# Performance work log

Measured on AMD Instinct MI355X. Metric: run time of the kernel, lower is better.

Reference implementation:

```python
import jax, jax.numpy as jnp
from jax import lax
import numpy as np

DIM = 384
HEADS = 8
SR = 2
B, D0, D1, D2 = 4, 16, 16, 16
N = 1 + D0 * D1 * D2


def setup_inputs() -> dict:
    key = jax.random.key(0)
    ks = jax.random.split(key, 8)
    s = 0.02
    return {
        "x": jax.random.normal(ks[0], (B, N, DIM), dtype=jnp.float32),
        "q_w": jax.random.normal(ks[1], (DIM, DIM), dtype=jnp.float32) * s,
        "kv_w": jax.random.normal(ks[2], (2 * DIM, DIM), dtype=jnp.float32) * s,
        "proj_w": jax.random.normal(ks[3], (DIM, DIM), dtype=jnp.float32) * s,
        "proj_b": jnp.zeros((DIM,), dtype=jnp.float32),
        "sr_w": jax.random.normal(ks[4], (DIM, 1, SR, SR, SR), dtype=jnp.float32) * s,  # depthwise (groups=dim)
        "sr_b": jnp.zeros((DIM,), dtype=jnp.float32),
        "ln_g": jnp.ones((DIM,), dtype=jnp.float32),
        "ln_b": jnp.zeros((DIM,), dtype=jnp.float32),
        "d0": D0, "d1": D1, "d2": D2,
    }


def reference(x, q_w, kv_w, proj_w, proj_b, sr_w, sr_b, ln_g, ln_b, d0, d1, d2):
    B_, N_, C = x.shape
    hd = C // HEADS
    scale = hd ** -0.5

    # q projection -> [B, H, N, hd]
    q = (x @ q_w.T).reshape(B_, N_, HEADS, hd).transpose(0, 2, 1, 3)

    # spatial reduction of patch tokens (keep CLS token)
    x_ = x[:, 1:].transpose(0, 2, 1).reshape(B_, C, d0, d1, d2)
    x_ = lax.conv_general_dilated(
        x_, sr_w, window_strides=(SR, SR, SR), padding="VALID",
        dimension_numbers=("NCDHW", "OIDHW", "NCDHW"), feature_group_count=C,
    ) + sr_b[None, :, None, None, None]
    x_ = x_.reshape(B_, C, -1).transpose(0, 2, 1)           # [B, M-1, C]
    x_ = jnp.concatenate([x[:, 0:1], x_], axis=1)            # [B, M, C]

    # LayerNorm (eps=1e-5)
    mu = jnp.mean(x_, axis=-1, keepdims=True)
    var = jnp.var(x_, axis=-1, keepdims=True)
    x_ = (x_ - mu) / jnp.sqrt(var + 1e-5) * ln_g + ln_b

    M = x_.shape[1]
    kv = (x_ @ kv_w.T).reshape(B_, M, 2, HEADS, hd).transpose(2, 0, 3, 1, 4)
    k, v = kv[0], kv[1]                                      # [B, H, M, hd]

    attn = jax.nn.softmax(jnp.einsum("bhnd,bhmd->bhnm", q, k) * scale, axis=-1)
    out = jnp.einsum("bhnm,bhmd->bhnd", attn, v)
    out = out.transpose(0, 2, 1, 3).reshape(B_, N_, C)
    return out @ proj_w.T + proj_b
```

## Files before the change

### kernel.cpp

```cpp
#include <hip/hip_runtime.h>

typedef unsigned short u16;
typedef unsigned int u32;
typedef __bf16 bf16x8 __attribute__((ext_vector_type(8)));
typedef float f32x4 __attribute__((ext_vector_type(4)));

#define NTOK 4097
#define MTOK 513
#define MPAD 544
#define KPAD 640
#define NPAD_Q 4224
#define ROWS_X 16512

__device__ __forceinline__ u16 f2bf(float f) {
  u32 u = __builtin_bit_cast(u32, f);
  u = u + 0x7FFFu + ((u >> 16) & 1u);
  return (u16)(u >> 16);
}
__device__ __forceinline__ u16 f2bf_fast(float f) {
  u32 u = __builtin_bit_cast(u32, f);
  return (u16)((u + 0x8000u) >> 16);
}

__device__ __forceinline__ void gld16(const u16* g, u16* l) {
  __builtin_amdgcn_global_load_lds((const __attribute__((address_space(1))) u32*)g,
                                   (__attribute__((address_space(3))) u32*)l, 16, 0, 0);
}

#define NQW  147456
#define NKVW 294912
#define NPW  147456
#define GQW  (NQW / 8)
#define GKVW (NKVW / 8)
#define GPW  (NPW / 8)
#define GW   (GQW + GKVW + GPW)
#define SRLN_BLOCKS (4 * MTOK)
#define CAST_BLOCKS 192

__global__ void pre_kernel(const float* __restrict__ x, const float* __restrict__ qw,
                           const float* __restrict__ kvw, const float* __restrict__ pw,
                           const float* __restrict__ srw, const float* __restrict__ srb,
                           const float* __restrict__ lng, const float* __restrict__ lnb,
                           u16* __restrict__ qwb, u16* __restrict__ kvwb, u16* __restrict__ pwb,
                           u16* __restrict__ xln) {
  if (blockIdx.x < SRLN_BLOCKS) {
    int c = threadIdx.x;
    int bm = blockIdx.x;
    int b = bm / MTOK, m = bm - b * MTOK;
    float v;
    if (m == 0) {
      v = x[(b * NTOK) * 384 + c];
    } else {
      int mo = m - 1;
      int oz = mo >> 6, oy = (mo >> 3) & 7, ox = mo & 7;
      float acc = srb[c];
#pragma unroll
      for (int dz = 0; dz < 2; dz++)
#pragma unroll
        for (int dy = 0; dy < 2; dy++)
#pragma unroll
          for (int dx = 0; dx < 2; dx++) {
            int tok = 1 + ((2 * oz + dz) * 256 + (2 * oy + dy) * 16 + (2 * ox + dx));
            acc += x[(b * NTOK + tok) * 384 + c] * srw[c * 8 + dz * 4 + dy * 2 + dx];
          }
      v = acc;
    }
    float s1 = v, s2 = v * v;
#pragma unroll
    for (int msk = 32; msk >= 1; msk >>= 1) {
      s1 += __shfl_xor(s1, msk);
      s2 += __shfl_xor(s2, msk);
    }
    __shared__ float r1[6], r2[6];
    int w = threadIdx.x >> 6, lane = threadIdx.x & 63;
    if (lane == 0) { r1[w] = s1; r2[w] = s2; }
    __syncthreads();
    float S1 = 0.f, S2 = 0.f;
#pragma unroll
    for (int i = 0; i < 6; i++) { S1 += r1[i]; S2 += r2[i]; }
    float mu = S1 * (1.0f / 384.0f);
    float var = S2 * (1.0f / 384.0f) - mu * mu;
    float y = (v - mu) * rsqrtf(var + 1e-5f) * lng[c] + lnb[c];
    xln[(b * MPAD + m) * 384 + c] = f2bf(y);
  } else {
    int idx = (blockIdx.x - SRLN_BLOCKS) * blockDim.x + threadIdx.x;
    int stride = (gridDim.x - SRLN_BLOCKS) * blockDim.x;
    for (int g = idx; g < GW; g += stride) {
      const float* s;
      u16* d;
      int off;
      if (g < GQW) { s = qw; d = qwb; off = g * 8; }
      else if (g < GQW + GKVW) { s = kvw; d = kvwb; off = (g - GQW) * 8; }
      else { s = pw; d = pwb; off = (g - GQW - GKVW) * 8; }
      float4 v0 = *(const float4*)(s + off);
      float4 v1 = *(const float4*)(s + off + 4);
      uint4 o;
      u16* p = (u16*)&o;
      p[0] = f2bf(v0.x); p[1] = f2bf(v0.y); p[2] = f2bf(v0.z); p[3] = f2bf(v0.w);
      p[4] = f2bf(v1.x); p[5] = f2bf(v1.y); p[6] = f2bf(v1.z); p[7] = f2bf(v1.w);
      *(uint4*)(d + off) = o;
    }
  }
}

__device__ __forceinline__ void gemm_core(u16* aLds, u16* bLds,
                                          const u16* __restrict__ A, const u16* __restrict__ W,
                                          int mode, size_t rbase, int c0,
                                          u16* __restrict__ o1, u16* __restrict__ o2,
                                          float* __restrict__ of, const float* __restrict__ bias) {
  int tid = threadIdx.x, w = tid >> 6, lane = tid & 63, q4 = lane >> 4, c16 = lane & 15;
  int wr = w >> 1, wc = w & 1;
  int x7 = c16 & 7;

  auto stageAB = [&](int kc, int buf) {
#pragma unroll
    for (int i = 0; i < 4; i++) {
      int s = (w * 4 + i) * 64 + lane;
      int row = s >> 3, chp = s & 7;
      int ch = chp ^ (row & 7);
      gld16(A + (rbase + row) * 384 + kc * 64 + ch * 8, &aLds[buf * 8192 + (w * 4 + i) * 512]);
    }
#pragma unroll
    for (int i = 0; i < 4; i++) {
      int s = (w * 4 + i) * 64 + lane;
      int row = s >> 3, chp = s & 7;
      int ch = chp ^ (row & 7);
      gld16(W + (size_t)(c0 + row) * 384 + kc * 64 + ch * 8, &bLds[buf * 8192 + (w * 4 + i) * 512]);
    }
  };
  stageAB(0, 0);
  __syncthreads();

  f32x4 acc[4][4];
#pragma unroll
  for (int mt = 0; mt < 4; mt++)
#pragma unroll
    for (int nt = 0; nt < 4; nt++) acc[mt][nt] = (f32x4){0, 0, 0, 0};

  for (int c = 0; c < 6; c++) {
    int cb = c & 1, nb = cb ^ 1;
    if (c < 5) stageAB(c + 1, nb);
#pragma unroll
    for (int ks = 0; ks < 2; ks++) {
      bf16x8 af[4], bf[4];
#pragma unroll
      for (int mt = 0; mt < 4; mt++)
        af[mt] = *(const bf16x8*)(&aLds[cb * 8192 + (wr * 64 + mt * 16 + c16) * 64 + ((ks * 4 + q4) ^ x7) * 8]);
#pragma unroll
      for (int nt = 0; nt < 4; nt++)
        bf[nt] = *(const bf16x8*)(&bLds[cb * 8192 + (wc * 64 + nt * 16 + c16) * 64 + ((ks * 4 + q4) ^ x7) * 8]);
#pragma unroll
      for (int mt = 0; mt < 4; mt++)
#pragma unroll
        for (int nt = 0; nt < 4; nt++)
          acc[mt][nt] = __builtin_amdgcn_mfma_f32_16x16x32_bf16(af[mt], bf[nt], acc[mt][nt], 0, 0, 0);
    }
    __syncthreads();
  }

#pragma unroll
  for (int mt = 0; mt < 4; mt++)
#pragma unroll
    for (int nt = 0; nt < 4; nt++) {
      int col = c0 + wc * 64 + nt * 16 + c16;
#pragma unroll
      for (int r = 0; r < 4; r++) {
        int R = (int)rbase + wr * 64 + mt * 16 + q4 * 4 + r;
        float val = acc[mt][nt][r];
        if (mode == 1) {
          int b = R / MPAD;
          int m = R - b * MPAD;
          if (col < 384) {
            int h = col / 48, d = col - h * 48;
            o1[((size_t)(b * 8 + h) * KPAD + m) * 64 + d] = f2bf(val);
          } else {
            int c2 = col - 384;
            int h = c2 / 48, d = c2 - h * 48;
            o2[((size_t)(b * 8 + h) * 48 + d) * KPAD + m] = f2bf(val);
          }
        } else {
          if (R < 4 * NTOK) of[(size_t)R * 384 + col] = val + bias[col];
        }
      }
    }
}

__device__ __forceinline__ void gemm_core_f32A(u16* aLds, u16* bLds,
                                               const float* __restrict__ X, const u16* __restrict__ W,
                                               size_t rbase, int c0, u16* __restrict__ o1) {
  int tid = threadIdx.x, w = tid >> 6, lane = tid & 63, q4 = lane >> 4, c16 = lane & 15;
  int wr = w >> 1, wc = w & 1;
  int x7 = c16 & 7;

  float4 ra[2][2];
  auto loadA2 = [&](int kc, int half) {
#pragma unroll
    for (int i = 0; i < 2; i++) {
      int idx2 = half * 2 + i;
      int s = (w * 4 + idx2) * 64 + lane;
      int row = s >> 3, chp = s & 7;
      int ch = chp ^ (row & 7);
      int ar = (int)rbase + row;
      if (ar > 16387) ar = 16387;
      const float* pa = X + (size_t)ar * 384 + kc * 64 + ch * 8;
      ra[i][0] = *(const float4*)pa;
      ra[i][1] = *(const float4*)(pa + 4);
    }
  };
  auto writeA2 = [&](int buf, int half) {
#pragma unroll
    for (int i = 0; i < 2; i++) {
      int idx2 = half * 2 + i;
      uint4 oa;
      u16* p = (u16*)&oa;
      p[0] = f2bf(ra[i][0].x); p[1] = f2bf(ra[i][0].y);
      p[2] = f2bf(ra[i][0].z); p[3] = f2bf(ra[i][0].w);
      p[4] = f2bf(ra[i][1].x); p[5] = f2bf(ra[i][1].y);
      p[6] = f2bf(ra[i][1].z); p[7] = f2bf(ra[i][1].w);
      *(uint4*)(&aLds[buf * 8192 + (w * 4 + idx2) * 512 + lane * 8]) = oa;
    }
  };
  auto stageB = [&](int kc, int buf) {
#pragma unroll
    for (int i = 0; i < 4; i++) {
      int s = (w * 4 + i) * 64 + lane;
      int row = s >> 3, chp = s & 7;
      int ch = chp ^ (row & 7);
      gld16(W + (size_t)(c0 + row) * 384 + kc * 64 + ch * 8, &bLds[buf * 8192 + (w * 4 + i) * 512]);
    }
  };

  loadA2(0, 0);
  stageB(0, 0);
  writeA2(0, 0);
  loadA2(0, 1);
  writeA2(0, 1);
  __syncthreads();

  f32x4 acc[4][4];
#pragma unroll
  for (int mt = 0; mt < 4; mt++)
#pragma unroll
    for (int nt = 0; nt < 4; nt++) acc[mt][nt] = (f32x4){0, 0, 0, 0};

  for (int c = 0; c < 6; c++) {
    int cb = c & 1, nb = cb ^ 1;
    if (c < 5) { loadA2(c + 1, 0); stageB(c + 1, nb); }
    {
      bf16x8 af[4], bf[4];
#pragma unroll
      for (int mt = 0; mt < 4; mt++)
        af[mt] = *(const bf16x8*)(&aLds[cb * 8192 + (wr * 64 + mt * 16 + c16) * 64 + ((0 + q4) ^ x7) * 8]);
#pragma unroll
      for (int nt = 0; nt < 4; nt++)
        bf[nt] = *(const bf16x8*)(&bLds[cb * 8192 + (wc * 64 + nt * 16 + c16) * 64 + ((0 + q4) ^ x7) * 8]);
#pragma unroll
      for (int mt = 0; mt < 4; mt++)
#pragma unroll
        for (int nt = 0; nt < 4; nt++)
          acc[mt][nt] = __builtin_amdgcn_mfma_f32_16x16x32_bf16(af[mt], bf[nt], acc[mt][nt], 0, 0, 0);
    }
    if (c < 5) { writeA2(nb, 0); loadA2(c + 1, 1); }
    {
      bf16x8 af[4], bf[4];
#pragma unroll
      for (int mt = 0; mt < 4; mt++)
        af[mt] = *(const bf16x8*)(&aLds[cb * 8192 + (wr * 64 + mt * 16 + c16) * 64 + ((4 + q4) ^ x7) * 8]);
#pragma unroll
      for (int nt = 0; nt < 4; nt++)
        bf[nt] = *(const bf16x8*)(&bLds[cb * 8192 + (wc * 64 + nt * 16 + c16) * 64 + ((4 + q4) ^ x7) * 8]);
#pragma unroll
      for (int mt = 0; mt < 4; mt++)
#pragma unroll
        for (int nt = 0; nt < 4; nt++)
          acc[mt][nt] = __builtin_amdgcn_mfma_f32_16x16x32_bf16(af[mt], bf[nt], acc[mt][nt], 0, 0, 0);
    }
    if (c < 5) writeA2(nb, 1);
    __syncthreads();
  }

#pragma unroll
  for (int mt = 0; mt < 4; mt++)
#pragma unroll
    for (int nt = 0; nt < 4; nt++) {
      int col = c0 + wc * 64 + nt * 16 + c16;
#pragma unroll
      for (int r = 0; r < 4; r++) {
        int R = (int)rbase + wr * 64 + mt * 16 + q4 * 4 + r;
        int b = R / NTOK;
        if (b >= 4) continue;
        int n = R - b * NTOK;
        int h = col / 48, d = col - h * 48;
        o1[((size_t)(b * 8 + h) * NPAD_Q + n) * 64 + d] =
            f2bf(acc[mt][nt][r] * 0.14433756729740643f);
      }
    }
}

__global__ __launch_bounds__(256) void gemm_qkv(const float* __restrict__ x, const u16* __restrict__ qwb,
                                                const u16* __restrict__ xlnb, const u16* __restrict__ kvwb,
                                                u16* __restrict__ qb, u16* __restrict__ kb2,
                                                u16* __restrict__ vtb) {
  __shared__ __align__(16) u16 aLds[2 * 128 * 64];
  __shared__ __align__(16) u16 bLds[2 * 128 * 64];
  int bx = blockIdx.x;
  if (bx < 387) {
    gemm_core_f32A(aLds, bLds, x, qwb, (size_t)(bx % 129) * 128, (bx / 129) * 128, qb);
  } else {
    int i = bx - 387;
    gemm_core(aLds, bLds, xlnb, kvwb, 1, (size_t)(i % 17) * 128, (i / 17) * 128,
              kb2, vtb, nullptr, nullptr);
  }
}

__global__ __launch_bounds__(256) void gemm_out(const u16* __restrict__ A, const u16* __restrict__ W,
                                                float* __restrict__ of, const float* __restrict__ bias) {
  __shared__ __align__(16) u16 aLds[2 * 128 * 64];
  __shared__ __align__(16) u16 bLds[2 * 128 * 64];
  gemm_core(aLds, bLds, A, W, 2, (size_t)blockIdx.x * 128, blockIdx.y * 128,
            nullptr, nullptr, of, bias);
}

__global__ __launch_bounds__(256, 4) void attn_kernel(const u16* __restrict__ qb,
                                                      const u16* __restrict__ kb,
                                                      const u16* __restrict__ vt,
                                                      u16* __restrict__ outb) {
  __shared__ __align__(16) u16 klds[2][64][64];
  __shared__ __align__(16) u16 vlds[2][48][64];
  __shared__ __align__(16) u16 plds[4][16][76];
  int tid = threadIdx.x, w = tid >> 6, lane = tid & 63, q4 = lane >> 4, c16 = lane & 15;
  int bh = blockIdx.x;
  int n0 = blockIdx.y * 128 + w * 32;
  int r7 = c16 & 7;

  const uint4* qp = (const uint4*)(qb + ((size_t)bh * NPAD_Q + n0 + c16) * 64);
  bf16x8 aq[2][2];
#pragma unroll
  for (int rg = 0; rg < 2; rg++) {
    aq[rg][0] = __builtin_bit_cast(bf16x8, qp[rg * 128 + q4]);
    aq[rg][1] = __builtin_bit_cast(bf16x8, qp[rg * 128 + 4 + q4]);
  }

  const u16* kbase = kb + (size_t)bh * KPAD * 64;
  const u16* vbase = vt + (size_t)bh * 48 * KPAD;

  auto stage = [&](int cn, int buf) {
#pragma unroll
    for (int i = 0; i < 2; i++) {
      int s = (w * 2 + i) * 64 + lane;
      int row = s >> 3, chp = s & 7;
      int ch = chp ^ (row & 7);
      gld16(kbase + (size_t)(cn * 64 + row) * 64 + ch * 8, &klds[buf][(w * 2 + i) * 8][0]);
    }
#pragma unroll
    for (int i = 0; i < 2; i++) {
      int blk = w * 2 + i;
      if (blk < 6) {
        int s = blk * 64 + lane;
        int row = s >> 3, chp = s & 7;
        int ch = chp ^ (row & 7);
        gld16(vbase + (size_t)row * KPAD + cn * 64 + ch * 8, &vlds[buf][blk * 8][0]);
      }
    }
  };

  stage(0, 0);
  __syncthreads();

  f32x4 o[2][3];
  float lsum[2][4];
#pragma unroll
  for (int rg = 0; rg < 2; rg++) {
#pragma unroll
    for (int nt = 0; nt < 3; nt++) o[rg][nt] = (f32x4){0, 0, 0, 0};
#pragma unroll
    for (int r = 0; r < 4; r++) lsum[rg][r] = 0.f;
  }

  for (int c = 0; c < 8; c++) {
    int cb = c & 1, nb = cb ^ 1;
    stage(c + 1, nb);

    f32x4 s[2][4];
#pragma unroll
    for (int rg = 0; rg < 2; rg++)
#pragma unroll
      for (int t = 0; t < 4; t++) s[rg][t] = (f32x4){0, 0, 0, 0};
#pragma unroll
    for (int t = 0; t < 4; t++) {
      const u16* krow = &klds[cb][t * 16 + c16][0];
      bf16x8 k0 = *(const bf16x8*)(krow + (q4 ^ r7) * 8);
      bf16x8 k1 = *(const bf16x8*)(krow + ((q4 ^ r7) ^ 4) * 8);
#pragma unroll
      for (int rg = 0; rg < 2; rg++) {
        s[rg][t] = __builtin_amdgcn_mfma_f32_16x16x32_bf16(aq[rg][0], k0, s[rg][t], 0, 0, 0);
        s[rg][t] = __builtin_amdgcn_mfma_f32_16x16x32_bf16(aq[rg][1], k1, s[rg][t], 0, 0, 0);
      }
    }
#pragma unroll
    for (int rg = 0; rg < 2; rg++)
#pragma unroll
      for (int t = 0; t < 4; t++)
#pragma unroll
        for (int r = 0; r < 4; r++) {
          float e = __expf(s[rg][t][r]);
          s[rg][t][r] = e;
          lsum[rg][r] += e;
        }
    bf16x8 afrag[2][2];
#pragma unroll
    for (int rg = 0; rg < 2; rg++) {
#pragma unroll
      for (int t = 0; t < 4; t++)
#pragma unroll
        for (int r = 0; r < 4; r++) plds[w][q4 * 4 + r][t * 16 + c16] = f2bf_fast(s[rg][t][r]);
#pragma unroll
      for (int kl = 0; kl < 2; kl++)
        afrag[rg][kl] = *(const bf16x8*)(&plds[w][c16][kl * 32 + q4 * 8]);
    }
#pragma unroll
    for (int kl = 0; kl < 2; kl++)
#pragma unroll
      for (int nt = 0; nt < 3; nt++) {
        const u16* vrow = &vlds[cb][nt * 16 + c16][0];
        bf16x8 bv = *(const bf16x8*)(vrow + ((kl * 4 + q4) ^ r7) * 8);
#pragma unroll
        for (int rg = 0; rg < 2; rg++)
          o[rg][nt] = __builtin_amdgcn_mfma_f32_16x16x32_bf16(afrag[rg][kl], bv, o[rg][nt], 0, 0, 0);
      }
    __syncthreads();
  }

  {
    f32x4 s4[2] = {{0, 0, 0, 0}, {0, 0, 0, 0}};
    const u16* krow = &klds[0][c16][0];
    bf16x8 k0 = *(const bf16x8*)(krow + (q4 ^ r7) * 8);
    bf16x8 k1 = *(const bf16x8*)(krow + ((q4 ^ r7) ^ 4) * 8);
#pragma unroll
    for (int rg = 0; rg < 2; rg++) {
      s4[rg] = __builtin_amdgcn_mfma_f32_16x16x32_bf16(aq[rg][0], k0, s4[rg], 0, 0, 0);
      s4[rg] = __builtin_amdgcn_mfma_f32_16x16x32_bf16(aq[rg][1], k1, s4[rg], 0, 0, 0);
    }
    bf16x8 afrag[2];
#pragma unroll
    for (int rg = 0; rg < 2; rg++) {
#pragma unroll
      for (int r = 0; r < 4; r++) {
        float e = (c16 == 0) ? __expf(s4[rg][r]) : 0.f;
        lsum[rg][r] += e;
        plds[w][q4 * 4 + r][c16] = f2bf_fast(e);
        plds[w][q4 * 4 + r][16 + c16] = 0;
      }
      afrag[rg] = *(const bf16x8*)(&plds[w][c16][q4 * 8]);
    }
#pragma unroll
    for (int nt = 0; nt < 3; nt++) {
      const u16* vrow = &vlds[0][nt * 16 + c16][0];
      bf16x8 bv = *(const bf16x8*)(vrow + (q4 ^ r7) * 8);
#pragma unroll
      for (int rg = 0; rg < 2; rg++)
        o[rg][nt] = __builtin_amdgcn_mfma_f32_16x16x32_bf16(afrag[rg], bv, o[rg][nt], 0, 0, 0);
    }
  }

  int b = bh >> 3, h = bh & 7;
#pragma unroll
  for (int rg = 0; rg < 2; rg++) {
    float inv[4];
#pragma unroll
    for (int r = 0; r < 4; r++) {
      float l = lsum[rg][r];
      l += __shfl_xor(l, 1);
      l += __shfl_xor(l, 2);
      l += __shfl_xor(l, 4);
      l += __shfl_xor(l, 8);
      inv[r] = 1.0f / l;
    }
#pragma unroll
    for (int nt = 0; nt < 3; nt++)
#pragma unroll
      for (int r = 0; r < 4; r++) {
        int n = n0 + rg * 16 + q4 * 4 + r;
        if (n < NTOK) outb[((size_t)(b * NTOK + n)) * 384 + h * 48 + nt * 16 + c16] = f2bf(o[rg][nt][r] * inv[r]);
      }
  }
}

extern "C" void kernel_launch(void* const* d_in, const int* in_sizes, int n_in,
                              void* d_out, int out_size, void* d_ws, size_t ws_size,
                              hipStream_t stream) {
  const float* x = (const float*)d_in[0];
  const float* q_w = (const float*)d_in[1];
  const float* kv_w = (const float*)d_in[2];
  const float* proj_w = (const float*)d_in[3];
  const float* proj_b = (const float*)d_in[4];
  const float* sr_w = (const float*)d_in[5];
  const float* sr_b = (const float*)d_in[6];
  const float* ln_g = (const float*)d_in[7];
  const float* ln_b = (const float*)d_in[8];
  float* out = (float*)d_out;

  u16* ws = (u16*)d_ws;
  u16* x_b = ws;
  u16* qw_b = x_b + (size_t)ROWS_X * 384;
  u16* kvw_b = qw_b + 147456;
  u16* pw_b = kvw_b + 294912;
  u16* q_b = pw_b + 147456;
  u16* xln_b = q_b + (size_t)32 * NPAD_Q * 64;
  u16* k_b = xln_b + (size_t)4 * MPAD * 384;
  u16* vt_b = k_b + (size_t)32 * KPAD * 64;
  u16* attn_b = x_b;


  pre_kernel<<<SRLN_BLOCKS + CAST_BLOCKS, 384, 0, stream>>>(x, q_w, kv_w, proj_w, sr_w, sr_b,
                                                            ln_g, ln_b, qw_b, kvw_b, pw_b, xln_b);
  gemm_qkv<<<489, 256, 0, stream>>>(x, qw_b, xln_b, kvw_b, q_b, k_b, vt_b);
  attn_kernel<<<dim3(32, 33), 256, 0, stream>>>(q_b, k_b, vt_b, attn_b);
  gemm_out<<<dim3(129, 3), 256, 0, stream>>>(attn_b, pw_b, out, proj_b);
}
```

Baseline: 177.3 us.

## Fuse spatial-reduction LayerNorm and weight casts into QKV GEMM kernel

Removes the separate pre-kernel by folding its work into the QKV launch. KV blocks now compute the spatial-reduction conv plus LayerNorm for their own 128-row tile, then run three KV GEMM tiles on it. The Q and KV GEMMs read fp32 weights and convert them to bf16 while staging into LDS, and a few extra blocks cast the projection weight. This drops one launch and the global round trip of the cast weights. In exchange each block converts weights redundantly, and the 34 KV blocks do serial SR+LN work followed by three GEMM tiles, which may leave them running well after the Q blocks finish.

```diff
diff --git a/kernel.cpp b/kernel.cpp
--- a/kernel.cpp
+++ b/kernel.cpp
@@ -27,79 +27,60 @@
                                    (__attribute__((address_space(3))) u32*)l, 16, 0, 0);
 }
 
-#define NQW  147456
-#define NKVW 294912
-#define NPW  147456
-#define GQW  (NQW / 8)
-#define GKVW (NKVW / 8)
-#define GPW  (NPW / 8)
-#define GW   (GQW + GKVW + GPW)
-#define SRLN_BLOCKS (4 * MTOK)
-#define CAST_BLOCKS 192
-
-__global__ void pre_kernel(const float* __restrict__ x, const float* __restrict__ qw,
-                           const float* __restrict__ kvw, const float* __restrict__ pw,
-                           const float* __restrict__ srw, const float* __restrict__ srb,
-                           const float* __restrict__ lng, const float* __restrict__ lnb,
-                           u16* __restrict__ qwb, u16* __restrict__ kvwb, u16* __restrict__ pwb,
-                           u16* __restrict__ xln) {
-  if (blockIdx.x < SRLN_BLOCKS) {
-    int c = threadIdx.x;
-    int bm = blockIdx.x;
-    int b = bm / MTOK, m = bm - b * MTOK;
-    float v;
-    if (m == 0) {
-      v = x[(b * NTOK) * 384 + c];
-    } else {
-      int mo = m - 1;
-      int oz = mo >> 6, oy = (mo >> 3) & 7, ox = mo & 7;
-      float acc = srb[c];
-#pragma unroll
-      for (int dz = 0; dz < 2; dz++)
-#pragma unroll
-        for (int dy = 0; dy < 2; dy++)
-#pragma unroll
-          for (int dx = 0; dx < 2; dx++) {
-            int tok = 1 + ((2 * oz + dz) * 256 + (2 * oy + dy) * 16 + (2 * ox + dx));
-            acc += x[(b * NTOK + tok) * 384 + c] * srw[c * 8 + dz * 4 + dy * 2 + dx];
-          }
-      v = acc;
-    }
-    float s1 = v, s2 = v * v;
+#define GPW  18432
+#define KV_BLOCKS 34
+#define Q_BLOCKS  387
+#define PW_BLOCKS 72
+
+__device__ __forceinline__ float srln_val(const float* __restrict__ x, const float* __restrict__ srw,
+                                          const float* __restrict__ srb, int b, int m, int c) {
+  if (m == 0) return x[(b * NTOK) * 384 + c];
+  int mo = m - 1;
+  int oz = mo >> 6, oy = (mo >> 3) & 7, ox = mo & 7;
+  float acc = srb[c];
+#pragma unroll
+  for (int dz = 0; dz < 2; dz++)
+#pragma unroll
+    for (int dy = 0; dy < 2; dy++)
+#pragma unroll
+      for (int dx = 0; dx < 2; dx++) {
+        int tok = 1 + ((2 * oz + dz) * 256 + (2 * oy + dy) * 16 + (2 * ox + dx));
+        acc += x[(b * NTOK + tok) * 384 + c] * srw[c * 8 + dz * 4 + dy * 2 + dx];
+      }
+  return acc;
+}
+
+__device__ __forceinline__ void srln_tile128(const float* __restrict__ x,
+                                             const float* __restrict__ srw, const float* __restrict__ srb,
+                                             const float* __restrict__ lng, const float* __restrict__ lnb,
+                                             int rbase, u16* __restrict__ xln) {
+  int tid = threadIdx.x, w = tid >> 6, lane = tid & 63;
+  int ch0 = lane * 6;
+  for (int jj = 0; jj < 32; jj++) {
+    int R = rbase + w * 32 + jj;
+    int b = R / MPAD, m = R - b * MPAD;
+    if (m >= MTOK) continue;
+    float vv[6];
+    float s1 = 0.f, s2 = 0.f;
+#pragma unroll
+    for (int k = 0; k < 6; k++) {
+      float v = srln_val(x, srw, srb, b, m, ch0 + k);
+      vv[k] = v;
+      s1 += v;
+      s2 += v * v;
+    }
 #pragma unroll
     for (int msk = 32; msk >= 1; msk >>= 1) {
       s1 += __shfl_xor(s1, msk);
       s2 += __shfl_xor(s2, msk);
     }
-    __shared__ float r1[6], r2[6];
-    int w = threadIdx.x >> 6, lane = threadIdx.x & 63;
-    if (lane == 0) { r1[w] = s1; r2[w] = s2; }
-    __syncthreads();
-    float S1 = 0.f, S2 = 0.f;
-#pragma unroll
-    for (int i = 0; i < 6; i++) { S1 += r1[i]; S2 += r2[i]; }
-    float mu = S1 * (1.0f / 384.0f);
-    float var = S2 * (1.0f / 384.0f) - mu * mu;
-    float y = (v - mu) * rsqrtf(var + 1e-5f) * lng[c] + lnb[c];
-    xln[(b * MPAD + m) * 384 + c] = f2bf(y);
-  } else {
-    int idx = (blockIdx.x - SRLN_BLOCKS) * blockDim.x + threadIdx.x;
-    int stride = (gridDim.x - SRLN_BLOCKS) * blockDim.x;
-    for (int g = idx; g < GW; g += stride) {
-      const float* s;
-      u16* d;
-      int off;
-      if (g < GQW) { s = qw; d = qwb; off = g * 8; }
-      else if (g < GQW + GKVW) { s = kvw; d = kvwb; off = (g - GQW) * 8; }
-      else { s = pw; d = pwb; off = (g - GQW - GKVW) * 8; }
-      float4 v0 = *(const float4*)(s + off);
-      float4 v1 = *(const float4*)(s + off + 4);
-      uint4 o;
-      u16* p = (u16*)&o;
-      p[0] = f2bf(v0.x); p[1] = f2bf(v0.y); p[2] = f2bf(v0.z); p[3] = f2bf(v0.w);
-      p[4] = f2bf(v1.x); p[5] = f2bf(v1.y); p[6] = f2bf(v1.z); p[7] = f2bf(v1.w);
-      *(uint4*)(d + off) = o;
-    }
+    float mu = s1 * (1.0f / 384.0f);
+    float var = s2 * (1.0f / 384.0f) - mu * mu;
+    float rs = rsqrtf(var + 1e-5f);
+    u16* dst = xln + (size_t)(b * MPAD + m) * 384 + ch0;
+#pragma unroll
+    for (int k = 0; k < 6; k++)
+      dst[k] = f2bf((vv[k] - mu) * rs * lng[ch0 + k] + lnb[ch0 + k]);
   }
 }
 
@@ -185,14 +166,14 @@
     }
 }
 
-__device__ __forceinline__ void gemm_core_f32A(u16* aLds, u16* bLds,
-                                               const float* __restrict__ X, const u16* __restrict__ W,
-                                               size_t rbase, int c0, u16* __restrict__ o1) {
+__device__ __forceinline__ void gemm_q_f32ab(u16* aLds, u16* bLds,
+                                             const float* __restrict__ X, const float* __restrict__ QW,
+                                             size_t rbase, int c0, u16* __restrict__ o1) {
   int tid = threadIdx.x, w = tid >> 6, lane = tid & 63, q4 = lane >> 4, c16 = lane & 15;
   int wr = w >> 1, wc = w & 1;
   int x7 = c16 & 7;
 
-  float4 ra[2][2];
+  float4 ra[2][2], rb[2][2];
   auto loadA2 = [&](int kc, int half) {
 #pragma unroll
     for (int i = 0; i < 2; i++) {
@@ -207,6 +188,18 @@
       ra[i][1] = *(const float4*)(pa + 4);
     }
   };
+  auto loadB2 = [&](int kc, int half) {
+#pragma unroll
+    for (int i = 0; i < 2; i++) {
+      int idx2 = half * 2 + i;
+      int s = (w * 4 + idx2) * 64 + lane;
+      int row = s >> 3, chp = s & 7;
+      int ch = chp ^ (row & 7);
+      const float* pb = QW + (size_t)(c0 + row) * 384 + kc * 64 + ch * 8;
+      rb[i][0] = *(const float4*)pb;
+      rb[i][1] = *(const float4*)(pb + 4);
+    }
+  };
   auto writeA2 = [&](int buf, int half) {
 #pragma unroll
     for (int i = 0; i < 2; i++) {
@@ -220,21 +213,24 @@
       *(uint4*)(&aLds[buf * 8192 + (w * 4 + idx2) * 512 + lane * 8]) = oa;
     }
   };
-  auto stageB = [&](int kc, int buf) {
-#pragma unroll
-    for (int i = 0; i < 4; i++) {
-      int s = (w * 4 + i) * 64 + lane;
-      int row = s >> 3, chp = s & 7;
-      int ch = chp ^ (row & 7);
-      gld16(W + (size_t)(c0 + row) * 384 + kc * 64 + ch * 8, &bLds[buf * 8192 + (w * 4 + i) * 512]);
-    }
-  };
-
-  loadA2(0, 0);
-  stageB(0, 0);
-  writeA2(0, 0);
-  loadA2(0, 1);
-  writeA2(0, 1);
+  auto writeB2 = [&](int buf, int half) {
+#pragma unroll
+    for (int i = 0; i < 2; i++) {
+      int idx2 = half * 2 + i;
+      uint4 ob;
+      u16* p = (u16*)&ob;
+      p[0] = f2bf(rb[i][0].x); p[1] = f2bf(rb[i][0].y);
+      p[2] = f2bf(rb[i][0].z); p[3] = f2bf(rb[i][0].w);
+      p[4] = f2bf(rb[i][1].x); p[5] = f2bf(rb[i][1].y);
+      p[6] = f2bf(rb[i][1].z); p[7] = f2bf(rb[i][1].w);
+      *(uint4*)(&bLds[buf * 8192 + (w * 4 + idx2) * 512 + lane * 8]) = ob;
+    }
+  };
+
+  loadA2(0, 0); loadB2(0, 0);
+  writeA2(0, 0); writeB2(0, 0);
+  loadA2(0, 1); loadB2(0, 1);
+  writeA2(0, 1); writeB2(0, 1);
   __syncthreads();
 
   f32x4 acc[4][4];
@@ -245,7 +241,7 @@
 
   for (int c = 0; c < 6; c++) {
     int cb = c & 1, nb = cb ^ 1;
-    if (c < 5) { loadA2(c + 1, 0); stageB(c + 1, nb); }
+    if (c < 5) { loadA2(c + 1, 0); loadB2(c + 1, 0); }
     {
       bf16x8 af[4], bf[4];
 #pragma unroll
@@ -260,7 +256,7 @@
         for (int nt = 0; nt < 4; nt++)
           acc[mt][nt] = __builtin_amdgcn_mfma_f32_16x16x32_bf16(af[mt], bf[nt], acc[mt][nt], 0, 0, 0);
     }
-    if (c < 5) { writeA2(nb, 0); loadA2(c + 1, 1); }
+    if (c < 5) { writeA2(nb, 0); writeB2(nb, 0); loadA2(c + 1, 1); loadB2(c + 1, 1); }
     {
       bf16x8 af[4], bf[4];
 #pragma unroll
@@ -275,7 +271,7 @@
         for (int nt = 0; nt < 4; nt++)
           acc[mt][nt] = __builtin_amdgcn_mfma_f32_16x16x32_bf16(af[mt], bf[nt], acc[mt][nt], 0, 0, 0);
     }
-    if (c < 5) writeA2(nb, 1);
+    if (c < 5) { writeA2(nb, 1); writeB2(nb, 1); }
     __syncthreads();
   }
 
@@ -297,19 +293,148 @@
     }
 }
 
-__global__ __launch_bounds__(256) void gemm_qkv(const float* __restrict__ x, const u16* __restrict__ qwb,
-                                                const u16* __restrict__ xlnb, const u16* __restrict__ kvwb,
-                                                u16* __restrict__ qb, u16* __restrict__ kb2,
-                                                u16* __restrict__ vtb) {
+__device__ __forceinline__ void gemm_kv_f32b(u16* aLds, u16* bLds,
+                                             const u16* A, const float* __restrict__ KVW,
+                                             size_t rbase, int c0,
+                                             u16* __restrict__ o1, u16* __restrict__ o2) {
+  int tid = threadIdx.x, w = tid >> 6, lane = tid & 63, q4 = lane >> 4, c16 = lane & 15;
+  int wr = w >> 1, wc = w & 1;
+  int x7 = c16 & 7;
+
+  auto stageA = [&](int kc, int buf) {
+#pragma unroll
+    for (int i = 0; i < 4; i++) {
+      int s = (w * 4 + i) * 64 + lane;
+      int row = s >> 3, chp = s & 7;
+      int ch = chp ^ (row & 7);
+      gld16(A + (rbase + row) * 384 + kc * 64 + ch * 8, &aLds[buf * 8192 + (w * 4 + i) * 512]);
+    }
+  };
+  float4 rb[2][2];
+  auto loadB2 = [&](int kc, int half) {
+#pragma unroll
+    for (int i = 0; i < 2; i++) {
+      int idx2 = half * 2 + i;
+      int s = (w * 4 + idx2) * 64 + lane;
+      int row = s >> 3, chp = s & 7;
+      int ch = chp ^ (row & 7);
+      const float* pb = KVW + (size_t)(c0 + row) * 384 + kc * 64 + ch * 8;
+      rb[i][0] = *(const float4*)pb;
+      rb[i][1] = *(const float4*)(pb + 4);
+    }
+  };
+  auto writeB2 = [&](int buf, int half) {
+#pragma unroll
+    for (int i = 0; i < 2; i++) {
+      int idx2 = half * 2 + i;
+      uint4 ob;
+      u16* p = (u16*)&ob;
+      p[0] = f2bf(rb[i][0].x); p[1] = f2bf(rb[i][0].y);
+      p[2] = f2bf(rb[i][0].z); p[3] = f2bf(rb[i][0].w);
+      p[4] = f2bf(rb[i][1].x); p[5] = f2bf(rb[i][1].y);
+      p[6] = f2bf(rb[i][1].z); p[7] = f2bf(rb[i][1].w);
+      *(uint4*)(&bLds[buf * 8192 + (w * 4 + idx2) * 512 + lane * 8]) = ob;
+    }
+  };
+
+  stageA(0, 0);
+  loadB2(0, 0); writeB2(0, 0);
+  loadB2(0, 1); writeB2(0, 1);
+  __syncthreads();
+
+  f32x4 acc[4][4];
+#pragma unroll
+  for (int mt = 0; mt < 4; mt++)
+#pragma unroll
+    for (int nt = 0; nt < 4; nt++) acc[mt][nt] = (f32x4){0, 0, 0, 0};
+
+  for (int c = 0; c < 6; c++) {
+    int cb = c & 1, nb = cb ^ 1;
+    if (c < 5) { stageA(c + 1, nb); loadB2(c + 1, 0); }
+    {
+      bf16x8 af[4], bf[4];
+#pragma unroll
+      for (int mt = 0; mt < 4; mt++)
+        af[mt] = *(const bf16x8*)(&aLds[cb * 8192 + (wr * 64 + mt * 16 + c16) * 64 + ((0 + q4) ^ x7) * 8]);
+#pragma unroll
+      for (int nt = 0; nt < 4; nt++)
+        bf[nt] = *(const bf16x8*)(&bLds[cb * 8192 + (wc * 64 + nt * 16 + c16) * 64 + ((0 + q4) ^ x7) * 8]);
+#pragma unroll
+      for (int mt = 0; mt < 4; mt++)
+#pragma unroll
+        for (int nt = 0; nt < 4; nt++)
+          acc[mt][nt] = __builtin_amdgcn_mfma_f32_16x16x32_bf16(af[mt], bf[nt], acc[mt][nt], 0, 0, 0);
+    }
+    if (c < 5) { writeB2(nb, 0); loadB2(c + 1, 1); }
+    {
+      bf16x8 af[4], bf[4];
+#pragma unroll
+      for (int mt = 0; mt < 4; mt++)
+        af[mt] = *(const bf16x8*)(&aLds[cb * 8192 + (wr * 64 + mt * 16 + c16) * 64 + ((4 + q4) ^ x7) * 8]);
+#pragma unroll
+      for (int nt = 0; nt < 4; nt++)
+        bf[nt] = *(const bf16x8*)(&bLds[cb * 8192 + (wc * 64 + nt * 16 + c16) * 64 + ((4 + q4) ^ x7) * 8]);
+#pragma unroll
+      for (int mt = 0; mt < 4; mt++)
+#pragma unroll
+        for (int nt = 0; nt < 4; nt++)
+          acc[mt][nt] = __builtin_amdgcn_mfma_f32_16x16x32_bf16(af[mt], bf[nt], acc[mt][nt], 0, 0, 0);
+    }
+    if (c < 5) writeB2(nb, 1);
+    __syncthreads();
+  }
+
+#pragma unroll
+  for (int mt = 0; mt < 4; mt++)
+#pragma unroll
+    for (int nt = 0; nt < 4; nt++) {
+      int col = c0 + wc * 64 + nt * 16 + c16;
+#pragma unroll
+      for (int r = 0; r < 4; r++) {
+        int R = (int)rbase + wr * 64 + mt * 16 + q4 * 4 + r;
+        float val = acc[mt][nt][r];
+        int b = R / MPAD;
+        int m = R - b * MPAD;
+        if (col < 384) {
+          int h = col / 48, d = col - h * 48;
+          o1[((size_t)(b * 8 + h) * KPAD + m) * 64 + d] = f2bf(val);
+        } else {
+          int c2 = col - 384;
+          int h = c2 / 48, d = c2 - h * 48;
+          o2[((size_t)(b * 8 + h) * 48 + d) * KPAD + m] = f2bf(val);
+        }
+      }
+    }
+}
+
+__global__ __launch_bounds__(256) void fused_qkv(
+    const float* __restrict__ x, const float* __restrict__ qw, const float* __restrict__ kvw,
+    const float* __restrict__ pw, const float* __restrict__ srw, const float* __restrict__ srb,
+    const float* __restrict__ lng, const float* __restrict__ lnb,
+    u16* __restrict__ qb, u16* __restrict__ kb, u16* __restrict__ vtb,
+    u16* xln, u16* __restrict__ pwb) {
   __shared__ __align__(16) u16 aLds[2 * 128 * 64];
   __shared__ __align__(16) u16 bLds[2 * 128 * 64];
   int bx = blockIdx.x;
-  if (bx < 387) {
-    gemm_core_f32A(aLds, bLds, x, qwb, (size_t)(bx % 129) * 128, (bx / 129) * 128, qb);
+  if (bx < KV_BLOCKS) {
+    int rt = bx >> 1, cg = bx & 1;
+    srln_tile128(x, srw, srb, lng, lnb, rt * 128, xln);
+    __syncthreads();
+    for (int t = 0; t < 3; t++)
+      gemm_kv_f32b(aLds, bLds, xln, kvw, (size_t)rt * 128, cg * 384 + t * 128, kb, vtb);
+  } else if (bx < KV_BLOCKS + Q_BLOCKS) {
+    int i = bx - KV_BLOCKS;
+    gemm_q_f32ab(aLds, bLds, x, qw, (size_t)(i % 129) * 128, (i / 129) * 128, qb);
   } else {
-    int i = bx - 387;
-    gemm_core(aLds, bLds, xlnb, kvwb, 1, (size_t)(i % 17) * 128, (i / 17) * 128,
-              kb2, vtb, nullptr, nullptr);
+    int g = (bx - KV_BLOCKS - Q_BLOCKS) * 256 + threadIdx.x;
+    int off = g * 8;
+    float4 v0 = *(const float4*)(pw + off);
+    float4 v1 = *(const float4*)(pw + off + 4);
+    uint4 o;
+    u16* p = (u16*)&o;
+    p[0] = f2bf(v0.x); p[1] = f2bf(v0.y); p[2] = f2bf(v0.z); p[3] = f2bf(v0.w);
+    p[4] = f2bf(v1.x); p[5] = f2bf(v1.y); p[6] = f2bf(v1.z); p[7] = f2bf(v1.w);
+    *(uint4*)(pwb + off) = o;
   }
 }
 
@@ -512,9 +637,8 @@
   u16* attn_b = x_b;
 
 
-  pre_kernel<<<SRLN_BLOCKS + CAST_BLOCKS, 384, 0, stream>>>(x, q_w, kv_w, proj_w, sr_w, sr_b,
-                                                            ln_g, ln_b, qw_b, kvw_b, pw_b, xln_b);
-  gemm_qkv<<<489, 256, 0, stream>>>(x, qw_b, xln_b, kvw_b, q_b, k_b, vt_b);
+  fused_qkv<<<KV_BLOCKS + Q_BLOCKS + PW_BLOCKS, 256, 0, stream>>>(
+      x, q_w, kv_w, proj_w, sr_w, sr_b, ln_g, ln_b, q_b, k_b, vt_b, xln_b, pw_b);
   attn_kernel<<<dim3(32, 33), 256, 0, stream>>>(q_b, k_b, vt_b, attn_b);
   gemm_out<<<dim3(129, 3), 256, 0, stream>>>(attn_b, pw_b, out, proj_b);
 }
```

Measured after the change: 308.0 us. +73.7%, slower.
